# Kernel optimization log

Hardware: AMD Instinct MI355X
Metric: run time of the kernel (lower is better)

The kernel has to match this reference:

```python
import jax, jax.numpy as jnp
import numpy as np

# SLAYER SRM-ALPHA neuron / simulation constants (from netParams)
THETA = 10.0      # spike threshold
TAU_SR = 10.0     # PSP (SRM) time constant
TAU_REF = 1.0     # refractory time constant
SCALE_REF = 2.0
TAU_RHO = 1.0     # surrogate-gradient width (unused in fwd)
SCALE_RHO = 1.0
TS = 1.0
K_SRM = 100       # truncation of alpha kernel (values < 1e-4 beyond this)
K_REF = 16

def _alpha_kernel(tau, K, mult):
    t = jnp.arange(K, dtype=jnp.float32) * TS
    return mult * (t / tau) * jnp.exp(1.0 - t / tau)

SRM_KERNEL = _alpha_kernel(TAU_SR, K_SRM, 1.0)                       # eps(t)
REF_KERNEL = _alpha_kernel(TAU_REF, K_REF, -2.0 * THETA * SCALE_REF)  # nu(t)

def heaviside(u):
    return (u >= THETA).astype(u.dtype)

def psp(x):
    # causal temporal convolution with SRM alpha kernel; x: (..., T)
    T = x.shape[-1]
    K = SRM_KERNEL.shape[0]
    flat = x.reshape(-1, 1, T)  # (N, C=1, T)
    out = jax.lax.conv_general_dilated(flat, SRM_KERNEL[::-1].reshape(1, 1, K),
                                       (1,), [(K - 1, 0)])
    return out.reshape(x.shape)

def spike(v):
    # SLAYER spike generation with refractory feedback; v: (..., T)
    refk = REF_KERNEL[1:]          # refractory affects strictly future steps
    L = refk.shape[0]
    vT = jnp.moveaxis(v, -1, 0)    # (T, ...)
    pend0 = jnp.zeros(vT.shape[1:] + (L,), v.dtype)  # pending refractory contributions
    def step(pend, vt):
        u = vt + pend[..., 0]
        s = heaviside(u)
        pend = jnp.concatenate([pend[..., 1:], jnp.zeros_like(pend[..., :1])], axis=-1) \
               + s[..., None] * refk
        return pend, s
    _, sT = jax.lax.scan(step, pend0, vT)
    return jnp.moveaxis(sT, 0, -1)

def conv_t(x, W, pad):
    # per-timestep 2D conv (slayer.conv uses Conv3d with kernel (k,k,1), no bias)
    B, C, H, Wd, T = x.shape
    xt = jnp.transpose(x, (0, 4, 1, 2, 3)).reshape(B * T, C, H, Wd)
    y = jax.lax.conv_general_dilated(xt, W, (1, 1), [(pad, pad), (pad, pad)])
    Co, Ho, Wo = y.shape[1:]
    return jnp.transpose(y.reshape(B, T, Co, Ho, Wo), (0, 2, 3, 4, 1))

def pool_t(x):
    # slayer.pool(2): 2x2 sum-pool with constant weight 1.1*theta per element
    s = jax.lax.reduce_window(x, 0.0, jax.lax.add, (1, 1, 2, 2, 1), (1, 1, 2, 2, 1), 'VALID')
    return s * (1.1 * THETA)

def _forward(spikeInput, W1, W2, W3, W4, Wfc):
    x = spike(conv_t(psp(spikeInput), W1, 1))   # (B,16,48,48,T)
    x = spike(pool_t(psp(x)))                   # (B,16,24,24,T)
    x = spike(conv_t(psp(x), W2, 1))            # (B,32,24,24,T)
    x = spike(pool_t(psp(x)))                   # (B,32,12,12,T)
    x = spike(conv_t(psp(x), W3, 1))            # (B,64,12,12,T)
    x = spike(pool_t(psp(x)))                   # (B,64,6,6,T)
    x = spike(conv_t(psp(x), W4, 1))            # (B,64,6,6,T)
    x = spike(jnp.einsum('bchwt,kchw->bkt', psp(x), Wfc))  # (B,10,T)
    return x

def setup_inputs():
    key = jax.random.key(0)
    ks = jax.random.split(key, 6)
    B, T = 4, 200
    spikeInput = (jax.random.uniform(ks[0], (B, 2, 50, 50, T)) < 0.05).astype(jnp.float32)
    W1 = 0.5 * jax.random.normal(ks[1], (16, 2, 5, 5), jnp.float32)
    W2 = 0.25 * jax.random.normal(ks[2], (32, 16, 3, 3), jnp.float32)
    W3 = 0.25 * jax.random.normal(ks[3], (64, 32, 3, 3), jnp.float32)
    W4 = 0.25 * jax.random.normal(ks[4], (64, 64, 3, 3), jnp.float32)
    Wfc = 0.1 * jax.random.normal(ks[5], (10, 64, 6, 6), jnp.float32)
    return {"spikeInput": spikeInput, "W1": W1, "W2": W2, "W3": W3, "W4": W4, "Wfc": Wfc}

def reference(spikeInput, W1, W2, W3, W4, Wfc):
    return _forward(spikeInput, W1, W2, W3, W4, Wfc)
```

## Files before the change

kernel.cpp:

```cpp
#include <hip/hip_runtime.h>
#include <math.h>


#define THETA 10.0f
#define RSTRIDE 204

__global__ void prep_kernel(const float* __restrict__ W1, const float* __restrict__ W2,
                            const float* __restrict__ W3, const float* __restrict__ W4,
                            float* HQ, float* rk,
                            float* wt1, float* wt2, float* wt3, float* wt4) {
    int i = blockIdx.x * 256 + threadIdx.x;
    if (i < 144) {
        int k = i - 15;
        float val = 0.0f;
        if (k >= 0 && k <= 99) {
            float tf = (float)k;
            float x = tf / 10.0f;
            val = x * (float)exp((double)(1.0f - x));
        }
        HQ[i] = val;
    } else if (i < 160) {
        int j = i - 144;
        if (j < 15) {
            float t = (float)(j + 1);
            rk[j] = (-40.0f * t) * (float)exp((double)(1.0f - t));
        }
    } else if (i < 960) {
        int j = i - 160, co = j / 50, tp = j % 50;
        wt1[tp * 16 + co] = W1[j];
    } else if (i < 5568) {
        int j = i - 960, co = j / 144, tp = j % 144;
        wt2[tp * 32 + co] = W2[j];
    } else if (i < 24000) {
        int j = i - 5568, co = j / 288, tp = j % 288;
        wt3[tp * 64 + co] = W3[j];
    } else if (i < 60864) {
        int j = i - 24000, co = j / 576, tp = j % 576;
        wt4[tp * 64 + co] = W4[j];
    }
}

#define FIR_STEP(A0, A1, A2, A3, qx, qy, qz, qw, hA, hB)  \
    A0 = fmaf(hA.x, qw, A0);                              \
    A1 = fmaf(hA.y, qw, A1);                              \
    A2 = fmaf(hA.z, qw, A2);                              \
    A3 = fmaf(hA.w, qw, A3);                              \
    A0 = fmaf(hA.y, qz, A0);                              \
    A1 = fmaf(hA.z, qz, A1);                              \
    A2 = fmaf(hA.w, qz, A2);                              \
    A3 = fmaf(hB.x, qz, A3);                              \
    A0 = fmaf(hA.z, qy, A0);                              \
    A1 = fmaf(hA.w, qy, A1);                              \
    A2 = fmaf(hB.x, qy, A2);                              \
    A3 = fmaf(hB.y, qy, A3);                              \
    A0 = fmaf(hA.w, qx, A0);                              \
    A1 = fmaf(hB.x, qx, A1);                              \
    A2 = fmaf(hB.y, qx, A2);                              \
    A3 = fmaf(hB.z, qx, A3);

#define SCAN4(XV, p, rk)                                          \
    {                                                             \
        float u_, sv_;                                            \
        u_ = XV.x + p[0]; sv_ = (u_ >= THETA) ? 1.0f : 0.0f;      \
        XV.x = sv_;                                               \
        _Pragma("unroll")                                         \
        for (int i_ = 0; i_ < 14; ++i_) p[i_] = fmaf(sv_, rk[i_], p[i_ + 1]); \
        p[14] = sv_ * rk[14];                                     \
        u_ = XV.y + p[0]; sv_ = (u_ >= THETA) ? 1.0f : 0.0f;      \
        XV.y = sv_;                                               \
        _Pragma("unroll")                                         \
        for (int i_ = 0; i_ < 14; ++i_) p[i_] = fmaf(sv_, rk[i_], p[i_ + 1]); \
        p[14] = sv_ * rk[14];                                     \
        u_ = XV.z + p[0]; sv_ = (u_ >= THETA) ? 1.0f : 0.0f;      \
        XV.z = sv_;                                               \
        _Pragma("unroll")                                         \
        for (int i_ = 0; i_ < 14; ++i_) p[i_] = fmaf(sv_, rk[i_], p[i_ + 1]); \
        p[14] = sv_ * rk[14];                                     \
        u_ = XV.w + p[0]; sv_ = (u_ >= THETA) ? 1.0f : 0.0f;      \
        XV.w = sv_;                                               \
        _Pragma("unroll")                                         \
        for (int i_ = 0; i_ < 14; ++i_) p[i_] = fmaf(sv_, rk[i_], p[i_ + 1]); \
        p[14] = sv_ * rk[14];                                     \
    }

__device__ __forceinline__ void fir_run2(const float* __restrict__ row,
                                         const float4* __restrict__ HQ4,
                                         int t0, int jend, float4 (&acc)[2]) {
    float4 A = HQ4[2], B = HQ4[3], C = HQ4[4];
    const float* bp = row + t0 + 4;
    for (int j = 0; j <= jend; ++j) {
        const float4 qv = *reinterpret_cast<const float4*>(bp);
        const float4 N = HQ4[j + 5];
        FIR_STEP(acc[0].x, acc[0].y, acc[0].z, acc[0].w,
                 qv.x, qv.y, qv.z, qv.w, A, B)
        FIR_STEP(acc[1].x, acc[1].y, acc[1].z, acc[1].w,
                 qv.x, qv.y, qv.z, qv.w, B, C)
        A = B; B = C; C = N;
        bp -= 4;
    }
}

__device__ static const signed char FIR_ITEMS[8][4] = {
    {24, 12, 8, -1}, {22, 21, 4, -1}, {20, 19, 3, -1}, {18, 17, 2, -1},
    {16, 15, 1, 0},  {13, 11, 5, -1}, {14, 10, 6, -1}, {23, 9, 7, -1}};

template <bool SCAN>
__global__ __launch_bounds__(512) void spikepsp_kernel(const float* __restrict__ in,
                                                       float* __restrict__ out,
                                                       const float* __restrict__ HQ,
                                                       const float* __restrict__ rkt,
                                                       int n) {
    __shared__ __align__(16) float tile[64 * RSTRIDE];
    const int l = threadIdx.x & 63;
    const int w = threadIdx.x >> 6;
    const int s0 = blockIdx.x * 64;
    for (int i = threadIdx.x; i < 3200; i += 512) {
        const int slot = i / 50, q = i - slot * 50;
        const int ser = s0 + slot;
        float4 v = make_float4(0.f, 0.f, 0.f, 0.f);
        if (ser < n) v = *reinterpret_cast<const float4*>(in + (long)ser * 200 + 4 * q);
        *reinterpret_cast<float4*>(&tile[slot * RSTRIDE + 4 * q]) = v;
    }
    __syncthreads();
    if (SCAN) {
        if (w == 0) {
            float rk[15];
            #pragma unroll
            for (int i = 0; i < 15; ++i) rk[i] = rkt[i];
            float p[15];
            #pragma unroll
            for (int i = 0; i < 15; ++i) p[i] = 0.0f;
            float* row = tile + l * RSTRIDE;
            for (int tq = 0; tq < 50; ++tq) {
                float4 xv = *reinterpret_cast<const float4*>(&row[4 * tq]);
                SCAN4(xv, p, rk)
                *reinterpret_cast<float4*>(&row[4 * tq]) = xv;
            }
        }
        __syncthreads();
    }
    const bool valid = (s0 + l) < n;
    const float* row = tile + l * RSTRIDE;
    const float4* HQ4 = reinterpret_cast<const float4*>(HQ);
    float* op = out + (long)(s0 + l) * 200;
    #pragma unroll
    for (int k = 0; k < 4; ++k) {
        const int id = FIR_ITEMS[w][k];
        if (id < 0) break;
        const int t0 = 8 * id;
        const int jend = ((2 * id < 25) ? 2 * id : 25) + 1;
        float4 acc[2];
        acc[0] = make_float4(0.f, 0.f, 0.f, 0.f);
        acc[1] = make_float4(0.f, 0.f, 0.f, 0.f);
        fir_run2(row, HQ4, t0, jend, acc);
        if (valid) {
            *reinterpret_cast<float4*>(op + t0) = acc[0];
            *reinterpret_cast<float4*>(op + t0 + 4) = acc[1];
        }
    }
}

__global__ __launch_bounds__(512) void spikepsppool_kernel(const float* __restrict__ in,
                                                           float* __restrict__ out,
                                                           const float* __restrict__ HQ,
                                                           const float* __restrict__ rkt,
                                                           int C, int HO, int WO) {
    __shared__ __align__(16) float tile[64 * RSTRIDE];
    __shared__ int sbase[64];
    const int l = threadIdx.x & 63;
    const int w = threadIdx.x >> 6;
    const int o0 = blockIdx.x * 16;
    const int H = 2 * HO, W = 2 * WO;
    if (threadIdx.x < 64) {
        const int oi = threadIdx.x >> 2, p = threadIdx.x & 3;
        const int o = o0 + oi;
        const int wo = o % WO; int tmp = o / WO;
        const int ho = tmp % HO; tmp /= HO;
        const int c = tmp % C; const int b = tmp / C;
        sbase[threadIdx.x] = ((b * C + c) * H + 2 * ho + (p >> 1)) * W + 2 * wo + (p & 1);
    }
    __syncthreads();
    for (int i = threadIdx.x; i < 3200; i += 512) {
        const int slot = i / 50, q = i - slot * 50;
        const float4 v = *reinterpret_cast<const float4*>(in + (long)sbase[slot] * 200 + 4 * q);
        *reinterpret_cast<float4*>(&tile[slot * RSTRIDE + 4 * q]) = v;
    }
    __syncthreads();
    if (w == 0) {
        float rk[15];
        #pragma unroll
        for (int i = 0; i < 15; ++i) rk[i] = rkt[i];
        float p[15];
        #pragma unroll
        for (int i = 0; i < 15; ++i) p[i] = 0.0f;
        float* row = tile + l * RSTRIDE;
        for (int tq = 0; tq < 50; ++tq) {
            float4 xv = *reinterpret_cast<const float4*>(&row[4 * tq]);
            SCAN4(xv, p, rk)
            *reinterpret_cast<float4*>(&row[4 * tq]) = xv;
        }
    }
    __syncthreads();
    const int qb = l & ~3;
    const float* row = tile + l * RSTRIDE;
    const float4* HQ4 = reinterpret_cast<const float4*>(HQ);
    float* op = out + (long)(o0 + (l >> 2)) * 200;
    auto qsum = [&](float v) -> float {
        const float v0 = __shfl(v, qb + 0);
        const float v1 = __shfl(v, qb + 1);
        const float v2 = __shfl(v, qb + 2);
        const float v3 = __shfl(v, qb + 3);
        return (((v0 + v1) + v2) + v3) * 11.0f;
    };
    #pragma unroll
    for (int k = 0; k < 4; ++k) {
        const int id = FIR_ITEMS[w][k];
        if (id < 0) break;
        const int t0 = 8 * id;
        const int jend = ((2 * id < 25) ? 2 * id : 25) + 1;
        float4 acc[2];
        acc[0] = make_float4(0.f, 0.f, 0.f, 0.f);
        acc[1] = make_float4(0.f, 0.f, 0.f, 0.f);
        fir_run2(row, HQ4, t0, jend, acc);
        #pragma unroll
        for (int d = 0; d < 2; ++d) {
            float4 r;
            r.x = qsum(acc[d].x); r.y = qsum(acc[d].y);
            r.z = qsum(acc[d].z); r.w = qsum(acc[d].w);
            if ((l & 3) == 0)
                *reinterpret_cast<float4*>(op + t0 + 4 * d) = r;
        }
    }
}

template <int K, int PAD, int CI, int COG>
__global__ __launch_bounds__(256) void conv_kernel(const float* __restrict__ x,
                                                   const float* __restrict__ wt,
                                                   float* __restrict__ out,
                                                   int Co, int H, int W,
                                                   int HO, int WO) {
    const int l = threadIdx.x & 63;
    const int wv = threadIdx.x >> 6;
    if (l >= 50) return;
    const int p = blockIdx.x * 4 + wv;
    const int wo = p % WO, ho = p / WO;
    const int co0 = blockIdx.y * COG;
    const int b = blockIdx.z;
    const int t0 = l * 4;
    float4 acc[COG];
    #pragma unroll
    for (int c = 0; c < COG; ++c) acc[c] = make_float4(0.f, 0.f, 0.f, 0.f);
    const float* xb = x + ((long)b * CI * H * W) * 200 + t0;
    for (int ci = 0; ci < CI; ++ci) {
        #pragma unroll
        for (int kh = 0; kh < K; ++kh) {
            const int hi = ho + kh - PAD;
            if (hi < 0 || hi >= H) continue;
            #pragma unroll
            for (int kw = 0; kw < K; ++kw) {
                const int wi = wo + kw - PAD;
                if (wi < 0 || wi >= W) continue;
                const float4 v = *reinterpret_cast<const float4*>(
                    xb + ((long)(ci * H + hi) * W + wi) * 200);
                const float* wp = wt + ((ci * K + kh) * K + kw) * Co + co0;
                #pragma unroll
                for (int c = 0; c < COG; ++c) {
                    const float wv_ = wp[c];
                    acc[c].x = fmaf(wv_, v.x, acc[c].x);
                    acc[c].y = fmaf(wv_, v.y, acc[c].y);
                    acc[c].z = fmaf(wv_, v.z, acc[c].z);
                    acc[c].w = fmaf(wv_, v.w, acc[c].w);
                }
            }
        }
    }
    const long hwN = (long)HO * WO;
    const long ob = ((long)(b * Co + co0) * HO + ho) * WO + wo;
    #pragma unroll
    for (int c = 0; c < COG; ++c)
        *reinterpret_cast<float4*>(out + (ob + c * hwN) * 200 + t0) = acc[c];
}

template <int CI, int COG>
__global__ __launch_bounds__(256) void conv3_kernel(const float* __restrict__ x,
                                                    const float* __restrict__ wt,
                                                    float* __restrict__ out,
                                                    int Co, int H, int W) {
    const int l = threadIdx.x & 63;
    const int wv = threadIdx.x >> 6;
    if (l >= 50) return;
    const int p = blockIdx.x * 4 + wv;
    const int wo = p % W, ho = p / W;
    const int co0 = blockIdx.y * COG;
    const int b = blockIdx.z;
    const int t0 = l * 4;
    float4 acc[COG];
    #pragma unroll
    for (int c = 0; c < COG; ++c) acc[c] = make_float4(0.f, 0.f, 0.f, 0.f);

    bool vm[9];
    #pragma unroll
    for (int i = 0; i < 9; ++i) {
        const int hi = ho + i / 3 - 1, wi = wo + i % 3 - 1;
        vm[i] = (hi >= 0) && (hi < H) && (wi >= 0) && (wi < W);
    }
    const long cis = (long)H * W * 200;
    const float* pb = x + (long)b * CI * cis + ((long)(ho - 1) * W + (wo - 1)) * 200 + t0;

    float4 bufA[9], bufB[9];
    auto ld = [&](int ci, float4 (&B)[9]) {
        const float* pc = pb + ci * cis;
        #pragma unroll
        for (int i = 0; i < 9; ++i) {
            B[i] = vm[i] ? *reinterpret_cast<const float4*>(pc + ((i / 3) * W + (i % 3)) * 200)
                         : make_float4(0.f, 0.f, 0.f, 0.f);
        }
    };
    auto fm = [&](const float4 (&B)[9], int ci) {
        #pragma unroll
        for (int i = 0; i < 9; ++i) {
            const float* wp = wt + (ci * 9 + i) * Co + co0;
            #pragma unroll
            for (int c = 0; c < COG; ++c) {
                const float wv_ = wp[c];
                acc[c].x = fmaf(wv_, B[i].x, acc[c].x);
                acc[c].y = fmaf(wv_, B[i].y, acc[c].y);
                acc[c].z = fmaf(wv_, B[i].z, acc[c].z);
                acc[c].w = fmaf(wv_, B[i].w, acc[c].w);
            }
        }
    };

    ld(0, bufA);
    #pragma unroll 1
    for (int ci = 0; ci < CI; ci += 2) {
        ld(ci + 1, bufB);
        fm(bufA, ci);
        if (ci + 2 < CI) ld(ci + 2, bufA);
        fm(bufB, ci + 1);
    }

    const long hwN = (long)H * W;
    const long ob = ((long)(b * Co + co0) * H + ho) * W + wo;
    #pragma unroll
    for (int c = 0; c < COG; ++c)
        *reinterpret_cast<float4*>(out + (ob + c * hwN) * 200 + t0) = acc[c];
}

__global__ __launch_bounds__(256) void spike_kernel(const float* __restrict__ v,
                                                    float* __restrict__ s,
                                                    const float* __restrict__ rkt,
                                                    int n) {
    const int nid = blockIdx.x * 256 + threadIdx.x;
    if (nid >= n) return;
    float rk[15];
    #pragma unroll
    for (int i = 0; i < 15; ++i) rk[i] = rkt[i];
    float p[15];
    #pragma unroll
    for (int i = 0; i < 15; ++i) p[i] = 0.0f;
    const float* vp = v + (long)nid * 200;
    float* sp = s + (long)nid * 200;
    for (int t = 0; t < 200; ++t) {
        const float u = vp[t] + p[0];
        const float sv = (u >= THETA) ? 1.0f : 0.0f;
        sp[t] = sv;
        #pragma unroll
        for (int i = 0; i < 14; ++i) p[i] = fmaf(sv, rk[i], p[i + 1]);
        p[14] = sv * rk[14];
    }
}

__global__ __launch_bounds__(128) void fc_kernel(const float* __restrict__ x,
                                                 const float* __restrict__ wf,
                                                 float* __restrict__ out) {
    __shared__ __align__(16) float xs[8 * 2308];
    const int b = blockIdx.x;
    const int t0 = blockIdx.y * 8;
    const int tid = threadIdx.x;
    const float* xb = x + (long)b * 2304 * 200 + t0;
    for (int i = tid; i < 4608; i += 128) {
        const int m = i >> 1, qh = (i & 1) * 4;
        const float4 v = *reinterpret_cast<const float4*>(xb + (long)m * 200 + qh);
        xs[(qh + 0) * 2308 + m] = v.x;
        xs[(qh + 1) * 2308 + m] = v.y;
        xs[(qh + 2) * 2308 + m] = v.z;
        xs[(qh + 3) * 2308 + m] = v.w;
    }
    __syncthreads();
    if (tid < 80) {
        const int k = tid >> 3, q = tid & 7;
        float a = 0.0f;
        const float* wp = wf + k * 2304;
        const float* xp = xs + q * 2308;
        for (int m4 = 0; m4 < 2304; m4 += 4) {
            const float4 xv = *reinterpret_cast<const float4*>(xp + m4);
            const float4 wv = *reinterpret_cast<const float4*>(wp + m4);
            a = fmaf(wv.x, xv.x, a);
            a = fmaf(wv.y, xv.y, a);
            a = fmaf(wv.z, xv.z, a);
            a = fmaf(wv.w, xv.w, a);
        }
        out[((long)b * 10 + k) * 200 + t0 + q] = a;
    }
}

extern "C" void kernel_launch(void* const* d_in, const int* in_sizes, int n_in,
                              void* d_out, int out_size, void* d_ws, size_t ws_size,
                              hipStream_t stream) {
    const float* x_in = (const float*)d_in[0];
    const float* W1 = (const float*)d_in[1];
    const float* W2 = (const float*)d_in[2];
    const float* W3 = (const float*)d_in[3];
    const float* W4 = (const float*)d_in[4];
    const float* Wfc = (const float*)d_in[5];
    float* outp = (float*)d_out;

    float* ws = (float*)d_ws;
    float* HQ  = ws;
    float* rk  = ws + 144;
    float* wt1 = ws + 160;
    float* wt2 = wt1 + 800;
    float* wt3 = wt2 + 4608;
    float* wt4 = wt3 + 18432;
    float* A   = wt4 + 36864;
    float* B   = A + 7372800;
    float* C   = B + 29491200;

    hipLaunchKernelGGL(prep_kernel, dim3(238), dim3(256), 0, stream,
                       W1, W2, W3, W4, HQ, rk, wt1, wt2, wt3, wt4);

    hipLaunchKernelGGL((spikepsp_kernel<false>), dim3(313), dim3(512), 0, stream,
                       x_in, A, HQ, rk, 20000);
    hipLaunchKernelGGL((conv_kernel<5, 1, 2, 16>), dim3(2304 / 4, 1, 4), dim3(256), 0, stream,
                       A, wt1, B, 16, 50, 50, 48, 48);
    hipLaunchKernelGGL(spikepsppool_kernel, dim3(36864 / 16), dim3(512), 0, stream,
                       B, A, HQ, rk, 16, 24, 24);
    hipLaunchKernelGGL((spikepsp_kernel<true>), dim3(36864 / 64), dim3(512), 0, stream,
                       A, B, HQ, rk, 36864);
    hipLaunchKernelGGL((conv3_kernel<16, 8>), dim3(576 / 4, 4, 4), dim3(256), 0, stream,
                       B, wt2, C, 32, 24, 24);
    hipLaunchKernelGGL(spikepsppool_kernel, dim3(18432 / 16), dim3(512), 0, stream,
                       C, A, HQ, rk, 32, 12, 12);
    hipLaunchKernelGGL((spikepsp_kernel<true>), dim3(18432 / 64), dim3(512), 0, stream,
                       A, B, HQ, rk, 18432);
    hipLaunchKernelGGL((conv3_kernel<32, 8>), dim3(144 / 4, 8, 4), dim3(256), 0, stream,
                       B, wt3, C, 64, 12, 12);
    hipLaunchKernelGGL(spikepsppool_kernel, dim3(9216 / 16), dim3(512), 0, stream,
                       C, A, HQ, rk, 64, 6, 6);
    hipLaunchKernelGGL((spikepsp_kernel<true>), dim3(9216 / 64), dim3(512), 0, stream,
                       A, B, HQ, rk, 9216);
    hipLaunchKernelGGL((conv3_kernel<64, 4>), dim3(36 / 4, 16, 4), dim3(256), 0, stream,
                       B, wt4, C, 64, 6, 6);
    hipLaunchKernelGGL((spikepsp_kernel<true>), dim3(9216 / 64), dim3(512), 0, stream,
                       C, B, HQ, rk, 9216);
    hipLaunchKernelGGL(fc_kernel, dim3(4, 25), dim3(128), 0, stream, B, Wfc, A);
    hipLaunchKernelGGL(spike_kernel, dim3(1), dim3(256), 0, stream, A, outp, rk, 40);
    (void)in_sizes; (void)n_in; (void)out_size; (void)ws_size;
}
```

Before: 675.9 us.

## Pipeline spike scan and PSP FIR across tiles with double-buffered persistent blocks

Replaces the one-tile-per-block spike+PSP and spike+pool+PSP kernels with persistent kernels that loop over tiles using two LDS buffers. Wave 0 runs the serial refractory scan on the next tile while the other seven waves compute the FIR on the current tile, and the FIR work is redistributed over seven waves. This aims to hide the serial scan, which previously idled seven of eight waves. The cost is a fixed grid of 256 blocks, double the shared memory per block (lower occupancy), and staging of later tiles that is no longer overlapped with compute.

```diff
diff --git a/kernel.cpp b/kernel.cpp
--- a/kernel.cpp
+++ b/kernel.cpp
@@ -39,24 +39,6 @@
         wt4[tp * 64 + co] = W4[j];
     }
 }
-
-#define FIR_STEP(A0, A1, A2, A3, qx, qy, qz, qw, hA, hB)  \
-    A0 = fmaf(hA.x, qw, A0);                              \
-    A1 = fmaf(hA.y, qw, A1);                              \
-    A2 = fmaf(hA.z, qw, A2);                              \
-    A3 = fmaf(hA.w, qw, A3);                              \
-    A0 = fmaf(hA.y, qz, A0);                              \
-    A1 = fmaf(hA.z, qz, A1);                              \
-    A2 = fmaf(hA.w, qz, A2);                              \
-    A3 = fmaf(hB.x, qz, A3);                              \
-    A0 = fmaf(hA.z, qy, A0);                              \
-    A1 = fmaf(hA.w, qy, A1);                              \
-    A2 = fmaf(hB.x, qy, A2);                              \
-    A3 = fmaf(hB.y, qy, A3);                              \
-    A0 = fmaf(hA.w, qx, A0);                              \
-    A1 = fmaf(hB.x, qx, A1);                              \
-    A2 = fmaf(hB.y, qx, A2);                              \
-    A3 = fmaf(hB.z, qx, A3);
 
 #define SCAN4(XV, p, rk)                                          \
     {                                                             \
@@ -83,6 +65,24 @@
         p[14] = sv_ * rk[14];                                     \
     }
 
+#define FIR_STEP(A0, A1, A2, A3, qx, qy, qz, qw, hA, hB)  \
+    A0 = fmaf(hA.x, qw, A0);                              \
+    A1 = fmaf(hA.y, qw, A1);                              \
+    A2 = fmaf(hA.z, qw, A2);                              \
+    A3 = fmaf(hA.w, qw, A3);                              \
+    A0 = fmaf(hA.y, qz, A0);                              \
+    A1 = fmaf(hA.z, qz, A1);                              \
+    A2 = fmaf(hA.w, qz, A2);                              \
+    A3 = fmaf(hB.x, qz, A3);                              \
+    A0 = fmaf(hA.z, qy, A0);                              \
+    A1 = fmaf(hA.w, qy, A1);                              \
+    A2 = fmaf(hB.x, qy, A2);                              \
+    A3 = fmaf(hB.y, qy, A3);                              \
+    A0 = fmaf(hA.w, qx, A0);                              \
+    A1 = fmaf(hB.x, qx, A1);                              \
+    A2 = fmaf(hB.y, qx, A2);                              \
+    A3 = fmaf(hB.z, qx, A3);
+
 __device__ __forceinline__ void fir_run2(const float* __restrict__ row,
                                          const float4* __restrict__ HQ4,
                                          int t0, int jend, float4 (&acc)[2]) {
@@ -100,16 +100,18 @@
     }
 }
 
-__device__ static const signed char FIR_ITEMS[8][4] = {
+__device__ static const signed char FIR_ITEMS8[8][4] = {
     {24, 12, 8, -1}, {22, 21, 4, -1}, {20, 19, 3, -1}, {18, 17, 2, -1},
     {16, 15, 1, 0},  {13, 11, 5, -1}, {14, 10, 6, -1}, {23, 9, 7, -1}};
 
-template <bool SCAN>
-__global__ __launch_bounds__(512) void spikepsp_kernel(const float* __restrict__ in,
-                                                       float* __restrict__ out,
-                                                       const float* __restrict__ HQ,
-                                                       const float* __restrict__ rkt,
-                                                       int n) {
+__device__ static const signed char FIR7[7][4] = {
+    {24, 23, 8, -1}, {22, 21, 7, 0}, {20, 19, 6, 1}, {18, 17, 5, 2},
+    {16, 15, 4, 3},  {14, 12, 10, -1}, {13, 11, 9, -1}};
+
+__global__ __launch_bounds__(512) void psp0_kernel(const float* __restrict__ in,
+                                                   float* __restrict__ out,
+                                                   const float* __restrict__ HQ,
+                                                   int n) {
     __shared__ __align__(16) float tile[64 * RSTRIDE];
     const int l = threadIdx.x & 63;
     const int w = threadIdx.x >> 6;
@@ -122,30 +124,13 @@
         *reinterpret_cast<float4*>(&tile[slot * RSTRIDE + 4 * q]) = v;
     }
     __syncthreads();
-    if (SCAN) {
-        if (w == 0) {
-            float rk[15];
-            #pragma unroll
-            for (int i = 0; i < 15; ++i) rk[i] = rkt[i];
-            float p[15];
-            #pragma unroll
-            for (int i = 0; i < 15; ++i) p[i] = 0.0f;
-            float* row = tile + l * RSTRIDE;
-            for (int tq = 0; tq < 50; ++tq) {
-                float4 xv = *reinterpret_cast<const float4*>(&row[4 * tq]);
-                SCAN4(xv, p, rk)
-                *reinterpret_cast<float4*>(&row[4 * tq]) = xv;
-            }
-        }
-        __syncthreads();
-    }
     const bool valid = (s0 + l) < n;
     const float* row = tile + l * RSTRIDE;
     const float4* HQ4 = reinterpret_cast<const float4*>(HQ);
     float* op = out + (long)(s0 + l) * 200;
     #pragma unroll
     for (int k = 0; k < 4; ++k) {
-        const int id = FIR_ITEMS[w][k];
+        const int id = FIR_ITEMS8[w][k];
         if (id < 0) break;
         const int t0 = 8 * id;
         const int jend = ((2 * id < 25) ? 2 * id : 25) + 1;
@@ -160,51 +145,129 @@
     }
 }
 
-__global__ __launch_bounds__(512) void spikepsppool_kernel(const float* __restrict__ in,
-                                                           float* __restrict__ out,
-                                                           const float* __restrict__ HQ,
-                                                           const float* __restrict__ rkt,
-                                                           int C, int HO, int WO) {
-    __shared__ __align__(16) float tile[64 * RSTRIDE];
-    __shared__ int sbase[64];
+__global__ __launch_bounds__(512) void psp_pipe_kernel(const float* __restrict__ in,
+                                                       float* __restrict__ out,
+                                                       const float* __restrict__ HQ,
+                                                       const float* __restrict__ rkt,
+                                                       int nt, int G) {
+    extern __shared__ __align__(16) float lds[];
     const int l = threadIdx.x & 63;
     const int w = threadIdx.x >> 6;
-    const int o0 = blockIdx.x * 16;
-    const int H = 2 * HO, W = 2 * WO;
-    if (threadIdx.x < 64) {
-        const int oi = threadIdx.x >> 2, p = threadIdx.x & 3;
-        const int o = o0 + oi;
-        const int wo = o % WO; int tmp = o / WO;
-        const int ho = tmp % HO; tmp /= HO;
-        const int c = tmp % C; const int b = tmp / C;
-        sbase[threadIdx.x] = ((b * C + c) * H + 2 * ho + (p >> 1)) * W + 2 * wo + (p & 1);
-    }
-    __syncthreads();
-    for (int i = threadIdx.x; i < 3200; i += 512) {
-        const int slot = i / 50, q = i - slot * 50;
-        const float4 v = *reinterpret_cast<const float4*>(in + (long)sbase[slot] * 200 + 4 * q);
-        *reinterpret_cast<float4*>(&tile[slot * RSTRIDE + 4 * q]) = v;
-    }
-    __syncthreads();
-    if (w == 0) {
-        float rk[15];
-        #pragma unroll
-        for (int i = 0; i < 15; ++i) rk[i] = rkt[i];
+    const int bid = blockIdx.x;
+    if (bid >= nt) return;
+    const int cnt = (nt - 1 - bid) / G + 1;
+    float* const buf0 = lds;
+    float* const buf1 = lds + 64 * RSTRIDE;
+    const float4* HQ4 = reinterpret_cast<const float4*>(HQ);
+    float rk[15];
+    #pragma unroll
+    for (int i = 0; i < 15; ++i) rk[i] = rkt[i];
+
+    auto stage = [&](float* dst, int t, int tid0, int stride) {
+        const float* src = in + (long)t * 64 * 200;
+        for (int i = tid0; i < 3200; i += stride) {
+            const int slot = i / 50, q = i - slot * 50;
+            *reinterpret_cast<float4*>(&dst[slot * RSTRIDE + 4 * q]) =
+                *reinterpret_cast<const float4*>(src + (long)slot * 200 + 4 * q);
+        }
+    };
+    auto scan = [&](float* b) {
         float p[15];
         #pragma unroll
         for (int i = 0; i < 15; ++i) p[i] = 0.0f;
-        float* row = tile + l * RSTRIDE;
+        float* row = b + l * RSTRIDE;
         for (int tq = 0; tq < 50; ++tq) {
             float4 xv = *reinterpret_cast<const float4*>(&row[4 * tq]);
             SCAN4(xv, p, rk)
             *reinterpret_cast<float4*>(&row[4 * tq]) = xv;
         }
-    }
+    };
+    auto fir = [&](const float* b, int t) {
+        const float* row = b + l * RSTRIDE;
+        float* op = out + ((long)t * 64 + l) * 200;
+        #pragma unroll
+        for (int k = 0; k < 4; ++k) {
+            const int id = FIR7[w - 1][k];
+            if (id < 0) break;
+            const int t0 = 8 * id;
+            const int jend = ((2 * id < 25) ? 2 * id : 25) + 1;
+            float4 acc[2];
+            acc[0] = make_float4(0.f, 0.f, 0.f, 0.f);
+            acc[1] = make_float4(0.f, 0.f, 0.f, 0.f);
+            fir_run2(row, HQ4, t0, jend, acc);
+            *reinterpret_cast<float4*>(op + t0) = acc[0];
+            *reinterpret_cast<float4*>(op + t0 + 4) = acc[1];
+        }
+    };
+
+    stage(buf0, bid, threadIdx.x, 512);
     __syncthreads();
+    if (w == 0) scan(buf0);
+    else if (cnt > 1) stage(buf1, bid + G, threadIdx.x - 64, 448);
+    __syncthreads();
+    for (int k = 0; k < cnt; ++k) {
+        float* cur = (k & 1) ? buf1 : buf0;
+        float* nxt = (k & 1) ? buf0 : buf1;
+        if (w == 0) {
+            if (k + 1 < cnt) scan(nxt);
+        } else {
+            fir(cur, bid + k * G);
+        }
+        __syncthreads();
+        if (k + 2 < cnt) {
+            stage(cur, bid + (k + 2) * G, threadIdx.x, 512);
+            __syncthreads();
+        }
+    }
+}
+
+template <int C, int HO, int WO>
+__global__ __launch_bounds__(512) void pool_pipe_kernel(const float* __restrict__ in,
+                                                        float* __restrict__ out,
+                                                        const float* __restrict__ HQ,
+                                                        const float* __restrict__ rkt,
+                                                        int nt, int G) {
+    extern __shared__ __align__(16) float lds[];
+    const int l = threadIdx.x & 63;
+    const int w = threadIdx.x >> 6;
+    const int bid = blockIdx.x;
+    if (bid >= nt) return;
+    const int cnt = (nt - 1 - bid) / G + 1;
+    float* const buf0 = lds;
+    float* const buf1 = lds + 64 * RSTRIDE;
+    const float4* HQ4 = reinterpret_cast<const float4*>(HQ);
+    float rk[15];
+    #pragma unroll
+    for (int i = 0; i < 15; ++i) rk[i] = rkt[i];
+
+    auto stage = [&](float* dst, int t, int tid0, int stride) {
+        const int o0 = t * 16;
+        for (int i = tid0; i < 3200; i += stride) {
+            const int slot = i / 50, q = i - slot * 50;
+            const int oi = slot >> 2, pq = slot & 3;
+            const int o = o0 + oi;
+            const int wo = o % WO;
+            const int ho = (o / WO) % HO;
+            const int c = (o / (WO * HO)) % C;
+            const int b = o / (WO * HO * C);
+            const long sb = ((long)((b * C + c) * (2 * HO) + 2 * ho + (pq >> 1))) * (2 * WO) +
+                            2 * wo + (pq & 1);
+            *reinterpret_cast<float4*>(&dst[slot * RSTRIDE + 4 * q]) =
+                *reinterpret_cast<const float4*>(in + sb * 200 + 4 * q);
+        }
+    };
+    auto scan = [&](float* b) {
+        float p[15];
+        #pragma unroll
+        for (int i = 0; i < 15; ++i) p[i] = 0.0f;
+        float* row = b + l * RSTRIDE;
+        for (int tq = 0; tq < 50; ++tq) {
+            float4 xv = *reinterpret_cast<const float4*>(&row[4 * tq]);
+            SCAN4(xv, p, rk)
+            *reinterpret_cast<float4*>(&row[4 * tq]) = xv;
+        }
+    };
     const int qb = l & ~3;
-    const float* row = tile + l * RSTRIDE;
-    const float4* HQ4 = reinterpret_cast<const float4*>(HQ);
-    float* op = out + (long)(o0 + (l >> 2)) * 200;
     auto qsum = [&](float v) -> float {
         const float v0 = __shfl(v, qb + 0);
         const float v1 = __shfl(v, qb + 1);
@@ -212,23 +275,47 @@
         const float v3 = __shfl(v, qb + 3);
         return (((v0 + v1) + v2) + v3) * 11.0f;
     };
-    #pragma unroll
-    for (int k = 0; k < 4; ++k) {
-        const int id = FIR_ITEMS[w][k];
-        if (id < 0) break;
-        const int t0 = 8 * id;
-        const int jend = ((2 * id < 25) ? 2 * id : 25) + 1;
-        float4 acc[2];
-        acc[0] = make_float4(0.f, 0.f, 0.f, 0.f);
-        acc[1] = make_float4(0.f, 0.f, 0.f, 0.f);
-        fir_run2(row, HQ4, t0, jend, acc);
-        #pragma unroll
-        for (int d = 0; d < 2; ++d) {
-            float4 r;
-            r.x = qsum(acc[d].x); r.y = qsum(acc[d].y);
-            r.z = qsum(acc[d].z); r.w = qsum(acc[d].w);
-            if ((l & 3) == 0)
-                *reinterpret_cast<float4*>(op + t0 + 4 * d) = r;
+    auto fir = [&](const float* b, int t) {
+        const float* row = b + l * RSTRIDE;
+        float* op = out + (long)(t * 16 + (l >> 2)) * 200;
+        #pragma unroll
+        for (int k = 0; k < 4; ++k) {
+            const int id = FIR7[w - 1][k];
+            if (id < 0) break;
+            const int t0 = 8 * id;
+            const int jend = ((2 * id < 25) ? 2 * id : 25) + 1;
+            float4 acc[2];
+            acc[0] = make_float4(0.f, 0.f, 0.f, 0.f);
+            acc[1] = make_float4(0.f, 0.f, 0.f, 0.f);
+            fir_run2(row, HQ4, t0, jend, acc);
+            #pragma unroll
+            for (int d = 0; d < 2; ++d) {
+                float4 r4;
+                r4.x = qsum(acc[d].x); r4.y = qsum(acc[d].y);
+                r4.z = qsum(acc[d].z); r4.w = qsum(acc[d].w);
+                if ((l & 3) == 0)
+                    *reinterpret_cast<float4*>(op + t0 + 4 * d) = r4;
+            }
+        }
+    };
+
+    stage(buf0, bid, threadIdx.x, 512);
+    __syncthreads();
+    if (w == 0) scan(buf0);
+    else if (cnt > 1) stage(buf1, bid + G, threadIdx.x - 64, 448);
+    __syncthreads();
+    for (int k = 0; k < cnt; ++k) {
+        float* cur = (k & 1) ? buf1 : buf0;
+        float* nxt = (k & 1) ? buf0 : buf1;
+        if (w == 0) {
+            if (k + 1 < cnt) scan(nxt);
+        } else {
+            fir(cur, bid + k * G);
+        }
+        __syncthreads();
+        if (k + 2 < cnt) {
+            stage(cur, bid + (k + 2) * G, threadIdx.x, 512);
+            __syncthreads();
         }
     }
 }
@@ -427,33 +514,47 @@
     float* B   = A + 7372800;
     float* C   = B + 29491200;
 
+    const int DYN = 2 * 64 * RSTRIDE * 4;
+    static bool attr_done = false;
+    if (!attr_done) {
+        hipFuncSetAttribute(reinterpret_cast<const void*>(&psp_pipe_kernel),
+                            hipFuncAttributeMaxDynamicSharedMemorySize, DYN);
+        hipFuncSetAttribute(reinterpret_cast<const void*>(&pool_pipe_kernel<16, 24, 24>),
+                            hipFuncAttributeMaxDynamicSharedMemorySize, DYN);
+        hipFuncSetAttribute(reinterpret_cast<const void*>(&pool_pipe_kernel<32, 12, 12>),
+                            hipFuncAttributeMaxDynamicSharedMemorySize, DYN);
+        hipFuncSetAttribute(reinterpret_cast<const void*>(&pool_pipe_kernel<64, 6, 6>),
+                            hipFuncAttributeMaxDynamicSharedMemorySize, DYN);
+        attr_done = true;
+    }
+
     hipLaunchKernelGGL(prep_kernel, dim3(238), dim3(256), 0, stream,
                        W1, W2, W3, W4, HQ, rk, wt1, wt2, wt3, wt4);
 
-    hipLaunchKernelGGL((spikepsp_kernel<false>), dim3(313), dim3(512), 0, stream,
-                       x_in, A, HQ, rk, 20000);
+    hipLaunchKernelGGL(psp0_kernel, dim3(313), dim3(512), 0, stream,
+                       x_in, A, HQ, 20000);
     hipLaunchKernelGGL((conv_kernel<5, 1, 2, 16>), dim3(2304 / 4, 1, 4), dim3(256), 0, stream,
                        A, wt1, B, 16, 50, 50, 48, 48);
-    hipLaunchKernelGGL(spikepsppool_kernel, dim3(36864 / 16), dim3(512), 0, stream,
-                       B, A, HQ, rk, 16, 24, 24);
-    hipLaunchKernelGGL((spikepsp_kernel<true>), dim3(36864 / 64), dim3(512), 0, stream,
-                       A, B, HQ, rk, 36864);
+    hipLaunchKernelGGL((pool_pipe_kernel<16, 24, 24>), dim3(256), dim3(512), DYN, stream,
+                       B, A, HQ, rk, 2304, 256);
+    hipLaunchKernelGGL(psp_pipe_kernel, dim3(256), dim3(512), DYN, stream,
+                       A, B, HQ, rk, 576, 256);
     hipLaunchKernelGGL((conv3_kernel<16, 8>), dim3(576 / 4, 4, 4), dim3(256), 0, stream,
                        B, wt2, C, 32, 24, 24);
-    hipLaunchKernelGGL(spikepsppool_kernel, dim3(18432 / 16), dim3(512), 0, stream,
-                       C, A, HQ, rk, 32, 12, 12);
-    hipLaunchKernelGGL((spikepsp_kernel<true>), dim3(18432 / 64), dim3(512), 0, stream,
-                       A, B, HQ, rk, 18432);
+    hipLaunchKernelGGL((pool_pipe_kernel<32, 12, 12>), dim3(256), dim3(512), DYN, stream,
+                       C, A, HQ, rk, 1152, 256);
+    hipLaunchKernelGGL(psp_pipe_kernel, dim3(256), dim3(512), DYN, stream,
+                       A, B, HQ, rk, 288, 256);
     hipLaunchKernelGGL((conv3_kernel<32, 8>), dim3(144 / 4, 8, 4), dim3(256), 0, stream,
                        B, wt3, C, 64, 12, 12);
-    hipLaunchKernelGGL(spikepsppool_kernel, dim3(9216 / 16), dim3(512), 0, stream,
-                       C, A, HQ, rk, 64, 6, 6);
-    hipLaunchKernelGGL((spikepsp_kernel<true>), dim3(9216 / 64), dim3(512), 0, stream,
-                       A, B, HQ, rk, 9216);
+    hipLaunchKernelGGL((pool_pipe_kernel<64, 6, 6>), dim3(256), dim3(512), DYN, stream,
+                       C, A, HQ, rk, 576, 256);
+    hipLaunchKernelGGL(psp_pipe_kernel, dim3(144), dim3(512), DYN, stream,
+                       A, B, HQ, rk, 144, 144);
     hipLaunchKernelGGL((conv3_kernel<64, 4>), dim3(36 / 4, 16, 4), dim3(256), 0, stream,
                        B, wt4, C, 64, 6, 6);
-    hipLaunchKernelGGL((spikepsp_kernel<true>), dim3(9216 / 64), dim3(512), 0, stream,
-                       C, B, HQ, rk, 9216);
+    hipLaunchKernelGGL(psp_pipe_kernel, dim3(144), dim3(512), DYN, stream,
+                       C, B, HQ, rk, 144, 144);
     hipLaunchKernelGGL(fc_kernel, dim3(4, 25), dim3(128), 0, stream, B, Wfc, A);
     hipLaunchKernelGGL(spike_kernel, dim3(1), dim3(256), 0, stream, A, outp, rk, 40);
     (void)in_sizes; (void)n_in; (void)out_size; (void)ws_size;
```

Measured after the change: 816.4 us. 1.21x slower.
